# Kernel tuning notes

Hardware: AMD Instinct MI355X
Metric: run time of the kernel (lower is better)

The kernel has to match this reference:

```python
import jax, jax.numpy as jnp
import numpy as np

SEQ = 8192
D_IN = 1024
D_OUT = 128


def setup_inputs() -> dict:
    key = jax.random.key(0)
    k0, k1, k2, k3 = jax.random.split(key, 4)
    # kaiming-normal-ish init for weights (std = sqrt(2/fan_in))
    std = np.sqrt(2.0 / D_IN).astype(np.float32)
    return {
        "x": jax.random.normal(k0, (SEQ, D_IN), dtype=jnp.float32),
        "wq": jax.random.normal(k1, (D_IN, D_OUT), dtype=jnp.float32) * std,
        "wk": jax.random.normal(k2, (D_IN, D_OUT), dtype=jnp.float32) * std,
        "wv": jax.random.normal(k3, (D_IN, D_OUT), dtype=jnp.float32) * std,
    }


def reference(x, wq, wk, wv):
    # q,k,v: [S, d_out]
    q = x @ wq
    k = x @ wk
    v = x @ wv
    scale = jnp.sqrt(jnp.asarray(D_OUT, dtype=q.dtype))
    scores = (q @ k.T) / scale          # [S, S]
    attn = jax.nn.softmax(scores, axis=-1)
    return attn @ v                      # [S, d_out]
```

## Files before the change

### kernel.cpp

```cpp
#include <hip/hip_runtime.h>
#include <cstdint>

#define SEQ    8192
#define DIN    1024
#define DOUT   128
#define NSPLIT 8
#define KVTILE 64
#define QTILE  128
#define QK_SCALE 0.1275174246f
#define RESCALE_THR 8.0f

typedef unsigned short u16;
typedef __bf16 bf16x8 __attribute__((ext_vector_type(8)));
typedef float  f32x4  __attribute__((ext_vector_type(4)));
typedef unsigned short u16x8 __attribute__((ext_vector_type(8)));
typedef unsigned short u16x4 __attribute__((ext_vector_type(4)));

__device__ __forceinline__ u16 bfc(float f) {
  return __builtin_bit_cast(u16, (__bf16)f);
}
__device__ __forceinline__ float bf2f(u16 u) {
  union { uint32_t u; float f; } c; c.u = ((uint32_t)u) << 16; return c.f;
}

__device__ __forceinline__ bf16x8 ldsu8(const u16* base, int byteoff) {
  return __builtin_bit_cast(bf16x8,
    *reinterpret_cast<const u16x8*>(reinterpret_cast<const char*>(base) + byteoff));
}
__device__ __forceinline__ bf16x8 glbu8(const u16* p) {
  return __builtin_bit_cast(bf16x8, *reinterpret_cast<const u16x8*>(p));
}

__device__ __forceinline__ void gload_lds16(const void* g, void* l) {
  __builtin_amdgcn_global_load_lds(
      (const __attribute__((address_space(1))) void*)g,
      (__attribute__((address_space(3))) void*)l, 16, 0, 0);
}

__global__ __launch_bounds__(256) void k_wtrans(const float* __restrict__ wq,
                                                const float* __restrict__ wk,
                                                const float* __restrict__ wv,
                                                u16* __restrict__ Wt) {
  const float* w = (blockIdx.y == 0) ? wq : (blockIdx.y == 1) ? wk : wv;
  int idx = blockIdx.x * 256 + threadIdx.x;
  int k = idx >> 7, n = idx & 127;
  Wt[(size_t)blockIdx.y * (DOUT * DIN) + (size_t)n * DIN + k] = bfc(w[idx]);
}

__global__ __launch_bounds__(256) void k_xcast(const float* __restrict__ x,
                                               u16* __restrict__ Xb) {
  size_t base = ((size_t)blockIdx.x * 256 + threadIdx.x) * 8;
  float4 lo = *reinterpret_cast<const float4*>(x + base);
  float4 hi = *reinterpret_cast<const float4*>(x + base + 4);
  u16x8 v = { bfc(lo.x), bfc(lo.y), bfc(lo.z), bfc(lo.w),
              bfc(hi.x), bfc(hi.y), bfc(hi.z), bfc(hi.w) };
  *reinterpret_cast<u16x8*>(Xb + base) = v;
}

__global__ __launch_bounds__(256, 2) void k_gemm(const u16* __restrict__ Xb,
                                                 const u16* __restrict__ Wt,
                                                 u16* __restrict__ Q,
                                                 u16* __restrict__ K,
                                                 u16* __restrict__ Vt) {
  __shared__ __attribute__((aligned(16))) u16 As[2][64 * 128];
  __shared__ __attribute__((aligned(16))) u16 Bs[2][96 * 128];
  const int tid  = threadIdx.x;
  const int lane = tid & 63, wave = tid >> 6;
  const int lm   = lane & 15, g = lane >> 4;
  const int wm   = wave >> 1, wn = wave & 1;
  const int m0   = blockIdx.x * 64;
  const int n0   = blockIdx.y * 96;
  const int swzr = (lm & 7) << 4;

  const int trow = tid >> 4;
  const int tswz = ((tid & 15) << 4) ^ ((trow & 7) << 4);
  const char* baseA = (const char*)Xb + (size_t)(m0 + trow) * 2048 + tswz;
  const char* baseB = (const char*)Wt + (size_t)(n0 + trow) * 2048 + tswz;

  auto stage = [&](int buf, int kc) {
    const int kb = kc * 256;
#pragma unroll
    for (int i = 0; i < 4; ++i)
      gload_lds16(baseA + kb + i * 32768, &As[buf][i * 2048 + wave * 512]);
#pragma unroll
    for (int j = 0; j < 6; ++j)
      gload_lds16(baseB + kb + j * 32768, &Bs[buf][j * 2048 + wave * 512]);
  };

  f32x4 acc[2][3];
#pragma unroll
  for (int s = 0; s < 2; ++s)
#pragma unroll
    for (int nb = 0; nb < 3; ++nb) acc[s][nb] = (f32x4){0.f, 0.f, 0.f, 0.f};

  auto compute = [&](int buf) {
    const u16* As_ = As[buf];
    const u16* Bs_ = Bs[buf];
    bf16x8 a[2][4], b[3][4];
#pragma unroll
    for (int s = 0; s < 2; ++s)
#pragma unroll
      for (int t = 0; t < 4; ++t)
        a[s][t] = ldsu8(As_, (wm * 32 + s * 16 + lm) * 256 +
                             ((t * 64 + 16 * g) ^ swzr));
#pragma unroll
    for (int nb = 0; nb < 3; ++nb)
#pragma unroll
      for (int t = 0; t < 4; ++t)
        b[nb][t] = ldsu8(Bs_, (wn * 48 + nb * 16 + lm) * 256 +
                              ((t * 64 + 16 * g) ^ swzr));
#pragma unroll
    for (int s = 0; s < 2; ++s)
#pragma unroll
      for (int nb = 0; nb < 3; ++nb)
#pragma unroll
        for (int t = 0; t < 4; ++t)
          acc[s][nb] = __builtin_amdgcn_mfma_f32_16x16x32_bf16(
              a[s][t], b[nb][t], acc[s][nb], 0, 0, 0);
  };

  stage(0, 0);
  asm volatile("s_waitcnt vmcnt(0)" ::: "memory");
  __syncthreads();

#pragma unroll
  for (int kc = 0; kc < 8; kc += 2) {
    if (kc + 1 < 8) stage(1, kc + 1);
    compute(0);
    asm volatile("s_waitcnt vmcnt(0)" ::: "memory");
    __syncthreads();
    if (kc + 2 < 8) stage(0, kc + 2);
    compute(1);
    asm volatile("s_waitcnt vmcnt(0)" ::: "memory");
    __syncthreads();
  }

#pragma unroll
  for (int s = 0; s < 2; ++s)
#pragma unroll
    for (int nb = 0; nb < 3; ++nb) {
      int n = n0 + wn * 48 + nb * 16 + lm;
      int which = n >> 7, col = n & 127;
#pragma unroll
      for (int r = 0; r < 4; ++r) {
        int m = m0 + wm * 32 + s * 16 + g * 4 + r;
        if (which == 0)       Q[(size_t)m * DOUT + col] = bfc(acc[s][nb][r] * QK_SCALE);
        else if (which == 1)  K[(size_t)m * DOUT + col] = bfc(acc[s][nb][r]);
        else                  Vt[(size_t)col * SEQ + m] = bfc(acc[s][nb][r]);
      }
    }
}

__global__ __launch_bounds__(512) void k_attn(const u16* __restrict__ Q,
                                              const u16* __restrict__ K,
                                              const u16* __restrict__ Vt,
                                              u16* __restrict__ Op,
                                              float* __restrict__ Mb,
                                              float* __restrict__ Lb) {
  __shared__ __attribute__((aligned(16))) u16 Ks[2][64 * 128];
  __shared__ __attribute__((aligned(16))) u16 Vts[2][128 * 64];
  __shared__ __attribute__((aligned(16))) u16 Ps[8][16 * 64];
  const int tid  = threadIdx.x;
  const int lane = tid & 63, wave = tid >> 6;
  const int lm   = lane & 15, g = lane >> 4;
  const int m0   = blockIdx.x * QTILE;
  const int split = blockIdx.y;
  const int kvbase = split * (SEQ / NSPLIT);
  const int NIT = (SEQ / NSPLIT) / KVTILE;

  auto stage = [&](int buf, int kv0) {
#pragma unroll
    for (int i = 0; i < 2; ++i) {
      int krow = wave * 8 + i * 4 + (lane >> 4);
      const char* gk = (const char*)K + ((size_t)(kv0 + krow) << 8) +
                       ((((lane & 15) << 4)) ^ ((krow & 7) << 4));
      gload_lds16(gk, &Ks[buf][wave * 1024 + i * 512]);
      int vrow = wave * 16 + i * 8 + (lane >> 3);
      const char* gv = (const char*)Vt + (size_t)vrow * (SEQ * 2) +
                       (size_t)kv0 * 2 +
                       ((((lane & 7) << 4)) ^ ((vrow & 7) << 4));
      gload_lds16(gv, &Vts[buf][wave * 1024 + i * 512]);
    }
  };

  bf16x8 qf[4];
  stage(0, kvbase);
  {
    const u16* qp = Q + (size_t)(m0 + wave * 16 + lm) * DOUT + 8 * g;
#pragma unroll
    for (int t = 0; t < 4; ++t) qf[t] = glbu8(qp + t * 32);
  }
  asm volatile("s_waitcnt vmcnt(0)" ::: "memory");
  __syncthreads();

  f32x4 o[8];
#pragma unroll
  for (int nb = 0; nb < 8; ++nb) o[nb] = (f32x4){0.f, 0.f, 0.f, 0.f};
  float mr = -1e30f, lr = 0.f;

  u16* pw = Ps[wave];
  char* pwb = reinterpret_cast<char*>(pw) + lm * 128;
  const int pswz = (lm & 7) << 4;
  int cur = 0;

  for (int it = 0; it < NIT; ++it) {
    if (it + 1 < NIT) stage(cur ^ 1, kvbase + (it + 1) * KVTILE);

    const u16* ks = Ks[cur];
    const u16* vs = Vts[cur];

    f32x4 s[4];
#pragma unroll
    for (int cb = 0; cb < 4; ++cb) {
      f32x4 a = (f32x4){0.f, 0.f, 0.f, 0.f};
      int krow = cb * 16 + lm;
#pragma unroll
      for (int t = 0; t < 4; ++t) {
        bf16x8 b = ldsu8(ks, krow * 256 +
                             (((t * 32 + 8 * g) * 2) ^ ((krow & 7) << 4)));
        a = __builtin_amdgcn_mfma_f32_16x16x32_bf16(b, qf[t], a, 0, 0, 0);
      }
      s[cb] = a;
    }

    float c0 = fmaxf(fmaxf(s[0][0], s[0][1]), fmaxf(s[0][2], s[0][3]));
    float c1 = fmaxf(fmaxf(s[1][0], s[1][1]), fmaxf(s[1][2], s[1][3]));
    float c2 = fmaxf(fmaxf(s[2][0], s[2][1]), fmaxf(s[2][2], s[2][3]));
    float c3 = fmaxf(fmaxf(s[3][0], s[3][1]), fmaxf(s[3][2], s[3][3]));
    float rm = fmaxf(fmaxf(c0, c1), fmaxf(c2, c3));
    rm = fmaxf(rm, __shfl_xor(rm, 16));
    rm = fmaxf(rm, __shfl_xor(rm, 32));

    if (__any(rm - mr > RESCALE_THR)) {
      float mn = fmaxf(mr, rm);
      float alpha = exp2f(mr - mn);
      mr = mn;
      lr *= alpha;
#pragma unroll
      for (int nb = 0; nb < 8; ++nb) o[nb] *= alpha;
    }

    float rsum = 0.f;
#pragma unroll
    for (int cb = 0; cb < 4; ++cb) {
      float p0 = exp2f(s[cb][0] - mr);
      float p1 = exp2f(s[cb][1] - mr);
      float p2 = exp2f(s[cb][2] - mr);
      float p3 = exp2f(s[cb][3] - mr);
      u16x4 w = { bfc(p0), bfc(p1), bfc(p2), bfc(p3) };
      *reinterpret_cast<u16x4*>(pwb + ((cb * 32 + g * 8) ^ pswz)) = w;
      rsum += (p0 + p1) + (p2 + p3);
    }
    rsum += __shfl_xor(rsum, 16);
    rsum += __shfl_xor(rsum, 32);
    lr += rsum;

    asm volatile("s_waitcnt lgkmcnt(0)" ::: "memory");
    __builtin_amdgcn_sched_barrier(0);

#pragma unroll
    for (int t = 0; t < 2; ++t) {
      bf16x8 pb = ldsu8(pw, lm * 128 + ((t * 64 + g * 16) ^ pswz));
#pragma unroll
      for (int nb = 0; nb < 8; ++nb) {
        int vrow = nb * 16 + lm;
        bf16x8 vb = ldsu8(vs, vrow * 128 +
                              (((t * 32 + 8 * g) * 2) ^ ((vrow & 7) << 4)));
        o[nb] = __builtin_amdgcn_mfma_f32_16x16x32_bf16(vb, pb, o[nb], 0, 0, 0);
      }
    }

    asm volatile("s_waitcnt vmcnt(0)" ::: "memory");
    __syncthreads();
    cur ^= 1;
  }

  const size_t ob = (size_t)split * SEQ * DOUT;
  const int m = m0 + wave * 16 + lm;
#pragma unroll
  for (int nb = 0; nb < 8; ++nb) {
    u16x4 w = { bfc(o[nb][0]), bfc(o[nb][1]), bfc(o[nb][2]), bfc(o[nb][3]) };
    *reinterpret_cast<u16x4*>(Op + ob + (size_t)m * DOUT + nb * 16 + g * 4) = w;
  }
  if (g == 0) {
    Mb[split * SEQ + m] = mr;
    Lb[split * SEQ + m] = lr;
  }
}

__global__ __launch_bounds__(256) void k_combine(const u16* __restrict__ Op,
                                                 const float* __restrict__ Mb,
                                                 const float* __restrict__ Lb,
                                                 float* __restrict__ out) {
  int idx = blockIdx.x * 256 + threadIdx.x;
  int srow = idx >> 7;
  float M = -1e30f;
#pragma unroll
  for (int s = 0; s < NSPLIT; ++s) M = fmaxf(M, Mb[s * SEQ + srow]);
  float num = 0.f, den = 0.f;
  const size_t st = (size_t)SEQ * DOUT;
#pragma unroll
  for (int s = 0; s < NSPLIT; ++s) {
    float e = exp2f(Mb[s * SEQ + srow] - M);
    den += Lb[s * SEQ + srow] * e;
    num += bf2f(Op[s * st + idx]) * e;
  }
  out[idx] = num / den;
}

extern "C" void kernel_launch(void* const* d_in, const int* in_sizes, int n_in,
                              void* d_out, int out_size, void* d_ws, size_t ws_size,
                              hipStream_t stream) {
  const float* x  = (const float*)d_in[0];
  const float* wq = (const float*)d_in[1];
  const float* wk = (const float*)d_in[2];
  const float* wv = (const float*)d_in[3];
  char* ws = (char*)d_ws;

  const size_t MB = (size_t)1 << 20;
  u16*   Wt = (u16*)(ws);
  u16*   Q  = (u16*)(ws + 768 * 1024);
  u16*   K  = (u16*)(ws + 768 * 1024 + 2 * MB);
  u16*   Vt = (u16*)(ws + 768 * 1024 + 4 * MB);
  float* Mb = (float*)(ws + 768 * 1024 + 6 * MB);
  float* Lb = (float*)(ws + 768 * 1024 + 6 * MB + 256 * 1024);
  u16*   Xb = (u16*)(ws + 7 * MB + 256 * 1024);
  u16*   Op = (u16*)(ws + 7 * MB + 256 * 1024);
  float* out = (float*)d_out;

  k_wtrans<<<dim3((DIN * DOUT) / 256, 3), 256, 0, stream>>>(wq, wk, wv, Wt);
  k_xcast<<<dim3((SEQ * DIN) / (256 * 8)), 256, 0, stream>>>(x, Xb);
  k_gemm<<<dim3(SEQ / 64, 4), 256, 0, stream>>>(Xb, Wt, Q, K, Vt);
  k_attn<<<dim3(SEQ / QTILE, NSPLIT), 512, 0, stream>>>(Q, K, Vt, Op, Mb, Lb);
  k_combine<<<dim3((SEQ * DOUT) / 256), 256, 0, stream>>>(Op, Mb, Lb, out);
}
```

Before: 92.23 us.

## Switch attention kernel to 32x32x16 MFMA with 4 waves of 32 query rows

Rewrites the flash-attention inner loop to use 32x32x16 bf16 MFMA instructions, with each of 4 waves owning 32 query rows instead of 8 waves owning 16. Row reductions now run mostly within a lane, since each lane holds a whole row's scores, so fewer cross-lane shuffles are needed. The grid is flattened so consecutive blocks share a query tile across splits, and s_setprio is raised around the MFMA sections. In exchange, accumulator register pressure per lane rises and each block carries fewer waves.

```diff
diff --git a/kernel.cpp b/kernel.cpp
--- a/kernel.cpp
+++ b/kernel.cpp
@@ -13,6 +13,7 @@
 typedef unsigned short u16;
 typedef __bf16 bf16x8 __attribute__((ext_vector_type(8)));
 typedef float  f32x4  __attribute__((ext_vector_type(4)));
+typedef float  f32x16 __attribute__((ext_vector_type(16)));
 typedef unsigned short u16x8 __attribute__((ext_vector_type(8)));
 typedef unsigned short u16x4 __attribute__((ext_vector_type(4)));
 
@@ -151,56 +152,55 @@
     }
 }
 
-__global__ __launch_bounds__(512) void k_attn(const u16* __restrict__ Q,
-                                              const u16* __restrict__ K,
-                                              const u16* __restrict__ Vt,
-                                              u16* __restrict__ Op,
-                                              float* __restrict__ Mb,
-                                              float* __restrict__ Lb) {
+__global__ __launch_bounds__(256, 2) void k_attn(const u16* __restrict__ Q,
+                                                 const u16* __restrict__ K,
+                                                 const u16* __restrict__ Vt,
+                                                 u16* __restrict__ Op,
+                                                 float* __restrict__ Mb,
+                                                 float* __restrict__ Lb) {
   __shared__ __attribute__((aligned(16))) u16 Ks[2][64 * 128];
   __shared__ __attribute__((aligned(16))) u16 Vts[2][128 * 64];
-  __shared__ __attribute__((aligned(16))) u16 Ps[8][16 * 64];
+  __shared__ __attribute__((aligned(16))) u16 Ps[4][32 * 64];
   const int tid  = threadIdx.x;
   const int lane = tid & 63, wave = tid >> 6;
-  const int lm   = lane & 15, g = lane >> 4;
-  const int m0   = blockIdx.x * QTILE;
-  const int split = blockIdx.y;
+  const int l31  = lane & 31, h = lane >> 5;
+  const int bid  = blockIdx.x;
+  const int split = bid & 7;
+  const int m0   = (bid >> 3) * QTILE;
   const int kvbase = split * (SEQ / NSPLIT);
   const int NIT = (SEQ / NSPLIT) / KVTILE;
 
   auto stage = [&](int buf, int kv0) {
 #pragma unroll
-    for (int i = 0; i < 2; ++i) {
-      int krow = wave * 8 + i * 4 + (lane >> 4);
+    for (int i = 0; i < 4; ++i) {
+      int krow = wave * 16 + i * 4 + (lane >> 4);
       const char* gk = (const char*)K + ((size_t)(kv0 + krow) << 8) +
-                       ((((lane & 15) << 4)) ^ ((krow & 7) << 4));
-      gload_lds16(gk, &Ks[buf][wave * 1024 + i * 512]);
-      int vrow = wave * 16 + i * 8 + (lane >> 3);
+                       (((lane & 15) << 4) ^ ((krow & 7) << 4));
+      gload_lds16(gk, &Ks[buf][wave * 2048 + i * 512]);
+      int vrow = wave * 32 + i * 8 + (lane >> 3);
       const char* gv = (const char*)Vt + (size_t)vrow * (SEQ * 2) +
                        (size_t)kv0 * 2 +
-                       ((((lane & 7) << 4)) ^ ((vrow & 7) << 4));
-      gload_lds16(gv, &Vts[buf][wave * 1024 + i * 512]);
+                       (((lane & 7) << 4) ^ ((vrow & 7) << 4));
+      gload_lds16(gv, &Vts[buf][wave * 2048 + i * 512]);
     }
   };
 
-  bf16x8 qf[4];
+  bf16x8 qf[8];
   stage(0, kvbase);
   {
-    const u16* qp = Q + (size_t)(m0 + wave * 16 + lm) * DOUT + 8 * g;
-#pragma unroll
-    for (int t = 0; t < 4; ++t) qf[t] = glbu8(qp + t * 32);
+    const u16* qp = Q + (size_t)(m0 + wave * 32 + l31) * DOUT + 8 * h;
+#pragma unroll
+    for (int t = 0; t < 8; ++t) qf[t] = glbu8(qp + t * 16);
   }
   asm volatile("s_waitcnt vmcnt(0)" ::: "memory");
   __syncthreads();
 
-  f32x4 o[8];
-#pragma unroll
-  for (int nb = 0; nb < 8; ++nb) o[nb] = (f32x4){0.f, 0.f, 0.f, 0.f};
+  f32x16 o[4] = {};
   float mr = -1e30f, lr = 0.f;
 
   u16* pw = Ps[wave];
-  char* pwb = reinterpret_cast<char*>(pw) + lm * 128;
-  const int pswz = (lm & 7) << 4;
+  char* pwb = reinterpret_cast<char*>(pw) + l31 * 128;
+  const int pswz = (l31 & 7) << 4;
   int cur = 0;
 
   for (int it = 0; it < NIT; ++it) {
@@ -209,26 +209,30 @@
     const u16* ks = Ks[cur];
     const u16* vs = Vts[cur];
 
-    f32x4 s[4];
-#pragma unroll
-    for (int cb = 0; cb < 4; ++cb) {
-      f32x4 a = (f32x4){0.f, 0.f, 0.f, 0.f};
-      int krow = cb * 16 + lm;
-#pragma unroll
-      for (int t = 0; t < 4; ++t) {
-        bf16x8 b = ldsu8(ks, krow * 256 +
-                             (((t * 32 + 8 * g) * 2) ^ ((krow & 7) << 4)));
-        a = __builtin_amdgcn_mfma_f32_16x16x32_bf16(b, qf[t], a, 0, 0, 0);
+    f32x16 s[2];
+    __builtin_amdgcn_s_setprio(1);
+#pragma unroll
+    for (int kb = 0; kb < 2; ++kb) {
+      f32x16 a = {};
+      int krow = kb * 32 + l31;
+      int rswz = (krow & 7) << 4;
+#pragma unroll
+      for (int t = 0; t < 8; ++t) {
+        bf16x8 kf = ldsu8(ks, krow * 256 + ((t * 32 + 16 * h) ^ rswz));
+        a = __builtin_amdgcn_mfma_f32_32x32x16_bf16(kf, qf[t], a, 0, 0, 0);
       }
-      s[cb] = a;
-    }
-
-    float c0 = fmaxf(fmaxf(s[0][0], s[0][1]), fmaxf(s[0][2], s[0][3]));
-    float c1 = fmaxf(fmaxf(s[1][0], s[1][1]), fmaxf(s[1][2], s[1][3]));
-    float c2 = fmaxf(fmaxf(s[2][0], s[2][1]), fmaxf(s[2][2], s[2][3]));
-    float c3 = fmaxf(fmaxf(s[3][0], s[3][1]), fmaxf(s[3][2], s[3][3]));
-    float rm = fmaxf(fmaxf(c0, c1), fmaxf(c2, c3));
-    rm = fmaxf(rm, __shfl_xor(rm, 16));
+      s[kb] = a;
+    }
+    __builtin_amdgcn_s_setprio(0);
+
+    float t8[8];
+#pragma unroll
+    for (int i = 0; i < 8; ++i)
+      t8[i] = fmaxf(fmaxf(s[0][2 * i], s[0][2 * i + 1]),
+                    fmaxf(s[1][2 * i], s[1][2 * i + 1]));
+    float u0 = fmaxf(fmaxf(t8[0], t8[1]), fmaxf(t8[2], t8[3]));
+    float u1 = fmaxf(fmaxf(t8[4], t8[5]), fmaxf(t8[6], t8[7]));
+    float rm = fmaxf(u0, u1);
     rm = fmaxf(rm, __shfl_xor(rm, 32));
 
     if (__any(rm - mr > RESCALE_THR)) {
@@ -237,54 +241,63 @@
       mr = mn;
       lr *= alpha;
 #pragma unroll
-      for (int nb = 0; nb < 8; ++nb) o[nb] *= alpha;
+      for (int db = 0; db < 4; ++db) o[db] *= alpha;
     }
 
     float rsum = 0.f;
 #pragma unroll
-    for (int cb = 0; cb < 4; ++cb) {
-      float p0 = exp2f(s[cb][0] - mr);
-      float p1 = exp2f(s[cb][1] - mr);
-      float p2 = exp2f(s[cb][2] - mr);
-      float p3 = exp2f(s[cb][3] - mr);
-      u16x4 w = { bfc(p0), bfc(p1), bfc(p2), bfc(p3) };
-      *reinterpret_cast<u16x4*>(pwb + ((cb * 32 + g * 8) ^ pswz)) = w;
-      rsum += (p0 + p1) + (p2 + p3);
-    }
-    rsum += __shfl_xor(rsum, 16);
-    rsum += __shfl_xor(rsum, 32);
+    for (int kb = 0; kb < 2; ++kb)
+#pragma unroll
+      for (int j = 0; j < 4; ++j) {
+        float p0 = exp2f(s[kb][4 * j + 0] - mr);
+        float p1 = exp2f(s[kb][4 * j + 1] - mr);
+        float p2 = exp2f(s[kb][4 * j + 2] - mr);
+        float p3 = exp2f(s[kb][4 * j + 3] - mr);
+        u16x4 w = { bfc(p0), bfc(p1), bfc(p2), bfc(p3) };
+        *reinterpret_cast<u16x4*>(pwb +
+            ((kb * 64 + 16 * j + 8 * h) ^ pswz)) = w;
+        rsum += (p0 + p1) + (p2 + p3);
+      }
     lr += rsum;
 
     asm volatile("s_waitcnt lgkmcnt(0)" ::: "memory");
     __builtin_amdgcn_sched_barrier(0);
 
-#pragma unroll
-    for (int t = 0; t < 2; ++t) {
-      bf16x8 pb = ldsu8(pw, lm * 128 + ((t * 64 + g * 16) ^ pswz));
-#pragma unroll
-      for (int nb = 0; nb < 8; ++nb) {
-        int vrow = nb * 16 + lm;
+    __builtin_amdgcn_s_setprio(1);
+#pragma unroll
+    for (int j = 0; j < 4; ++j) {
+      bf16x8 pb = ldsu8(pw, l31 * 128 + ((32 * j + 16 * h) ^ pswz));
+#pragma unroll
+      for (int db = 0; db < 4; ++db) {
+        int vrow = db * 32 + l31;
         bf16x8 vb = ldsu8(vs, vrow * 128 +
-                              (((t * 32 + 8 * g) * 2) ^ ((vrow & 7) << 4)));
-        o[nb] = __builtin_amdgcn_mfma_f32_16x16x32_bf16(vb, pb, o[nb], 0, 0, 0);
+                              ((32 * j + 16 * h) ^ ((vrow & 7) << 4)));
+        o[db] = __builtin_amdgcn_mfma_f32_32x32x16_bf16(vb, pb, o[db], 0, 0, 0);
       }
     }
+    __builtin_amdgcn_s_setprio(0);
 
     asm volatile("s_waitcnt vmcnt(0)" ::: "memory");
     __syncthreads();
     cur ^= 1;
   }
 
+  lr += __shfl_xor(lr, 32);
+
   const size_t ob = (size_t)split * SEQ * DOUT;
-  const int m = m0 + wave * 16 + lm;
-#pragma unroll
-  for (int nb = 0; nb < 8; ++nb) {
-    u16x4 w = { bfc(o[nb][0]), bfc(o[nb][1]), bfc(o[nb][2]), bfc(o[nb][3]) };
-    *reinterpret_cast<u16x4*>(Op + ob + (size_t)m * DOUT + nb * 16 + g * 4) = w;
-  }
-  if (g == 0) {
-    Mb[split * SEQ + m] = mr;
-    Lb[split * SEQ + m] = lr;
+  const int q = m0 + wave * 32 + l31;
+#pragma unroll
+  for (int db = 0; db < 4; ++db)
+#pragma unroll
+    for (int j = 0; j < 4; ++j) {
+      u16x4 w = { bfc(o[db][4 * j + 0]), bfc(o[db][4 * j + 1]),
+                  bfc(o[db][4 * j + 2]), bfc(o[db][4 * j + 3]) };
+      *reinterpret_cast<u16x4*>(Op + ob + (size_t)q * DOUT +
+                                db * 32 + 8 * j + 4 * h) = w;
+    }
+  if (h == 0) {
+    Mb[split * SEQ + q] = mr;
+    Lb[split * SEQ + q] = lr;
   }
 }
 
@@ -331,6 +344,6 @@
   k_wtrans<<<dim3((DIN * DOUT) / 256, 3), 256, 0, stream>>>(wq, wk, wv, Wt);
   k_xcast<<<dim3((SEQ * DIN) / (256 * 8)), 256, 0, stream>>>(x, Xb);
   k_gemm<<<dim3(SEQ / 64, 4), 256, 0, stream>>>(Xb, Wt, Q, K, Vt);
-  k_attn<<<dim3(SEQ / QTILE, NSPLIT), 512, 0, stream>>>(Q, K, Vt, Op, Mb, Lb);
+  k_attn<<<dim3((SEQ / QTILE) * NSPLIT), 256, 0, stream>>>(Q, K, Vt, Op, Mb, Lb);
   k_combine<<<dim3((SEQ * DOUT) / 256), 256, 0, stream>>>(Op, Mb, Lb, out);
 }
```

After: 90.91 us. Within noise of the previous version (-1.4%).
